# Kernel optimization log

Hardware: AMD Instinct MI355X
Metric: run time of the kernel (lower is better)

## Reference

```python
import jax, jax.numpy as jnp
import numpy as np
import math

B, N, EPG = 64, 1000, 16000          # graphs, nodes/graph, edges/graph
F_IN, H1, H2, C = 128, 128, 64, 10
RATIO = 0.8
K_PROP = 2


def setup_inputs():
    key = jax.random.key(0)
    ks = jax.random.split(key, 24)
    x = jax.random.normal(ks[0], (B * N, F_IN), jnp.float32)
    # edges generated within each graph, then offset to global node ids
    e = jax.random.randint(ks[1], (2, B, EPG), 0, N, dtype=jnp.int32)
    e = e + (jnp.arange(B, dtype=jnp.int32) * N)[None, :, None]
    out = {"x": x, "src": e[0].reshape(-1), "dst": e[1].reshape(-1)}

    def lin(k, fan_in, fan_out):
        s = 1.0 / math.sqrt(fan_in)
        kw, kb = jax.random.split(k)
        return (jax.random.uniform(kw, (fan_in, fan_out), jnp.float32, -s, s),
                jax.random.uniform(kb, (fan_out,), jnp.float32, -s, s))

    dims = [("11", F_IN, H1), ("12", F_IN, H1), ("13", F_IN, H1),
            ("21", H1, H1), ("22", H1, H1), ("23", H1, H1),
            ("31", H1, H1), ("32", H1, H1), ("33", H1, H1),
            ("1", 2 * H1, H1), ("2", H1, H2), ("3", H2, C)]
    for i, (nm, di, do) in enumerate(dims):
        w, b = lin(ks[2 + i], di, do)
        out["w" + nm] = w
        out["b" + nm] = b
    for i in range(3):
        out["p%d" % (i + 1)] = jax.random.normal(ks[20 + i], (H1,), jnp.float32)
    return out


def gcn_prop(h, src, dst, emask, n):
    # GCN symmetric norm with self-loops; emask zeroes filtered edges
    deg = jnp.zeros((n,), h.dtype).at[dst].add(emask) + 1.0
    dinv = jax.lax.rsqrt(deg)
    coef = dinv[src] * dinv[dst] * emask                      # [E]
    out = jnp.zeros_like(h).at[dst].add(h[src] * coef[:, None])
    return out + h * (dinv * dinv)[:, None]                   # self-loop term


def gra_inc(h, src, dst, emask):
    # Gra_inc(K): K incremental propagation steps h <- h + A_hat h
    for _ in range(K_PROP):
        h = h + gcn_prop(h, src, dst, emask, h.shape[0])
    return h


def topk_pool(x, src, dst, emask, p, n_per_graph):
    # PyG TopKPooling: score = x.p/||p||, keep top ceil(ratio*n) per graph,
    # gate kept features by tanh(score), filter & remap edges.
    k = int(math.ceil(RATIO * n_per_graph))
    score = x @ p / jnp.linalg.norm(p)                        # [B*n]
    idx = jax.lax.top_k(score.reshape(B, n_per_graph), k)[1]  # [B,k] local
    perm = (idx + (jnp.arange(B, dtype=idx.dtype) * n_per_graph)[:, None]).reshape(-1)
    new_x = x[perm] * jnp.tanh(score[perm])[:, None]
    remap = jnp.full((B * n_per_graph,), -1, jnp.int32).at[perm].set(
        jnp.arange(B * k, dtype=jnp.int32))
    ns, nd = remap[src], remap[dst]
    valid = emask * ((ns >= 0) & (nd >= 0)).astype(x.dtype)
    return new_x, jnp.maximum(ns, 0), jnp.maximum(nd, 0), valid, k


def readout(x, k):
    xg = x.reshape(B, k, H1)
    return jnp.concatenate([xg.max(axis=1), xg.mean(axis=1)], axis=-1)  # [B,2H]


def reference(x, src, dst, w11, b11, w12, b12, w13, b13, w21, b21, w22, b22,
              w23, b23, w31, b31, w32, b32, w33, b33, w1, b1, w2, b2, w3, b3,
              p1, p2, p3):
    emask = jnp.ones((src.shape[0],), x.dtype)
    n = N
    reads = []
    for (wa, ba), (wb, bb), (wc, bc), p in [
            ((w11, b11), (w12, b12), (w13, b13), p1),
            ((w21, b21), (w22, b22), (w23, b23), p2),
            ((w31, b31), (w32, b32), (w33, b33), p3)]:
        h = (gra_inc(jax.nn.relu(x @ wa + ba), src, dst, emask)
             + gra_inc(jax.nn.relu(x @ wb + bb), src, dst, emask)
             + gra_inc(jax.nn.relu(x @ wc + bc), src, dst, emask))
        x, src, dst, emask, n = topk_pool(h, src, dst, emask, p, n)
        reads.append(readout(x, n))
    z = reads[0] + reads[1] + reads[2]
    z = jax.nn.relu(z @ w1 + b1)
    z = jax.nn.relu(z @ w2 + b2)  # dropout identity in eval mode
    return jax.nn.log_softmax(z @ w3 + b3, axis=-1)
```

## Files before the change

### kernel.cpp

```cpp
#include <hip/hip_runtime.h>
#include <hip/hip_bf16.h>
#include <math.h>

#define BGR 64
#define ECAP 16000
#define EMAX 1024000

typedef _Float16 f16x8 __attribute__((ext_vector_type(8)));
typedef float f32x4 __attribute__((ext_vector_type(4)));

__global__ __launch_bounds__(128) void pnorm3_kernel(const float* __restrict__ p1,
                              const float* __restrict__ p2,
                              const float* __restrict__ p3, float* __restrict__ out) {
    __shared__ float buf[128];
    int t = threadIdx.x, b = blockIdx.x;
    const float* p = (b == 0) ? p1 : (b == 1) ? p2 : p3;
    buf[t] = p[t] * p[t];
    __syncthreads();
    for (int off = 64; off; off >>= 1) {
        if (t < off) buf[t] += buf[t + off];
        __syncthreads();
    }
    if (t == 0) out[b] = sqrtf(buf[0]);
}

struct WP { const float* w[9]; };

__global__ void wsplit_kernel(WP wp, _Float16* __restrict__ out) {
    int mat = blockIdx.x;
    const float* __restrict__ w = wp.w[mat];
    _Float16* __restrict__ dst = out + (size_t)mat * 32768;
    for (int e = threadIdx.x; e < 2048; e += 256) {
        int n = e >> 4;
        int kb = (e & 15) * 8;
        f16x8 hi, lo;
#pragma unroll
        for (int j = 0; j < 8; j++) {
            float v = w[(kb + j) * 128 + n];
            _Float16 h = (_Float16)v;
            hi[j] = h;
            lo[j] = (_Float16)((v - (float)h) * 2048.0f);
        }
        int ks = kb >> 5, kg = (kb >> 3) & 3;
        *(f16x8*)(dst + ((((ks * 2 + 0) * 4 + kg) * 128 + n) * 8)) = hi;
        *(f16x8*)(dst + ((((ks * 2 + 1) * 4 + kg) * 128 + n) * 8)) = lo;
    }
}

__global__ __launch_bounds__(1024) void build_kernel(
    const int* __restrict__ src, const int* __restrict__ dst,
    const int* __restrict__ gcnt, int fixedcnt, int npg,
    int2* __restrict__ rowdeg, float* __restrict__ dinv, int2* __restrict__ edata) {
    __shared__ int cnt[1024];
    __shared__ int scn[1024];
    __shared__ float sdinv[1024];
    int g = blockIdx.x, t = threadIdx.x;
    int E = gcnt ? gcnt[g] : fixedcnt;
    int ebase = g * ECAP;
    int gnb = g * npg;
    cnt[t] = 0;
    __syncthreads();
    for (int i = t; i < E; i += 1024)
        atomicAdd(&cnt[dst[ebase + i] - gnb], 1);
    __syncthreads();
    int myc = (t < npg) ? cnt[t] : 0;
    scn[t] = myc;
    __syncthreads();
    for (int off = 1; off < 1024; off <<= 1) {
        int v = (t >= off) ? scn[t - off] : 0;
        __syncthreads();
        scn[t] += v;
        __syncthreads();
    }
    int excl = scn[t] - myc;
    if (t < npg) {
        float dv = rsqrtf((float)myc + 1.0f);
        rowdeg[gnb + t] = make_int2(ebase + excl, myc);
        dinv[gnb + t] = dv;
        sdinv[t] = dv;
        scn[t] = excl;
    }
    __syncthreads();
    for (int i = t; i < E; i += 1024) {
        int s = src[ebase + i];
        int d = dst[ebase + i];
        int sl = s - gnb, dl = d - gnb;
        int pos = atomicAdd(&scn[dl], 1);
        edata[ebase + pos] = make_int2(s, __float_as_int(sdinv[sl] * sdinv[dl]));
    }
}

__global__ __launch_bounds__(256) void gemm3m_kernel(
    const float* __restrict__ x, const _Float16* __restrict__ wsp,
    const float* __restrict__ b0, const float* __restrict__ b1, const float* __restrict__ b2,
    float* __restrict__ out) {
    __shared__ _Float16 ws[2][16384] __attribute__((aligned(16)));
    const int tid = threadIdx.x;
    const int wave = tid >> 6;
    const int lane = tid & 63;
    const int l15 = lane & 15;
    const int kg = lane >> 4;
    const long base = (long)blockIdx.x * 64;
    const int m = wave * 16 + l15;

    float4 xrow[8];
    const float4* xg = (const float4*)(x + (base + m) * 128);
#pragma unroll
    for (int q = 0; q < 8; q++) xrow[q] = xg[(q >> 1) * 8 + kg * 2 + (q & 1)];

    auto stageH = [&](int s, int buf) {
#pragma unroll
        for (int t = 0; t < 8; t++) {
            int u = tid + t * 256;
            __builtin_amdgcn_global_load_lds(
                (const __attribute__((address_space(1))) unsigned int*)(wsp + (size_t)s * 16384 + u * 8),
                (__attribute__((address_space(3))) unsigned int*)(&ws[buf][u * 8]),
                16, 0, 0);
        }
    };

    float tot[8][4];
#pragma unroll
    for (int nt = 0; nt < 8; nt++)
#pragma unroll
        for (int r = 0; r < 4; r++) tot[nt][r] = 0.f;

    f32x4 acc_h[8], acc_m[8];
    stageH(0, 0);

    for (int s = 0; s < 6; s++) {
        const int j = s >> 1;
        __syncthreads();
        if (s < 5) stageH(s + 1, (s & 1) ^ 1);

        if ((s & 1) == 0) {
#pragma unroll
            for (int nt = 0; nt < 8; nt++) {
                acc_h[nt] = (f32x4){0.f, 0.f, 0.f, 0.f};
                acc_m[nt] = (f32x4){0.f, 0.f, 0.f, 0.f};
            }
        }

        const _Float16* wbase = &ws[s & 1][0];
#pragma unroll
        for (int ksl = 0; ksl < 2; ksl++) {
            const int ks = (s & 1) * 2 + ksl;
            float ev[8] = {xrow[ks * 2].x, xrow[ks * 2].y, xrow[ks * 2].z, xrow[ks * 2].w,
                           xrow[ks * 2 + 1].x, xrow[ks * 2 + 1].y, xrow[ks * 2 + 1].z, xrow[ks * 2 + 1].w};
            f16x8 ah, al;
#pragma unroll
            for (int i = 0; i < 8; i++) {
                _Float16 h = (_Float16)ev[i];
                ah[i] = h;
                al[i] = (_Float16)((ev[i] - (float)h) * 2048.0f);
            }
            const _Float16* wb = wbase + ksl * 8192;
            const int nb = kg * 1024 + l15 * 8;
            f16x8 bh[8], bl[8];
#pragma unroll
            for (int nt = 0; nt < 8; nt++) {
                bh[nt] = *(const f16x8*)(wb + nb + nt * 128);
                bl[nt] = *(const f16x8*)(wb + 4096 + nb + nt * 128);
            }
#pragma unroll
            for (int nt = 0; nt < 8; nt++)
                acc_h[nt] = __builtin_amdgcn_mfma_f32_16x16x32_f16(ah, bh[nt], acc_h[nt], 0, 0, 0);
#pragma unroll
            for (int nt = 0; nt < 8; nt++)
                acc_m[nt] = __builtin_amdgcn_mfma_f32_16x16x32_f16(ah, bl[nt], acc_m[nt], 0, 0, 0);
#pragma unroll
            for (int nt = 0; nt < 8; nt++)
                acc_m[nt] = __builtin_amdgcn_mfma_f32_16x16x32_f16(al, bh[nt], acc_m[nt], 0, 0, 0);
        }

        if (s & 1) {
            const float* bb = (j == 0) ? b0 : (j == 1) ? b1 : b2;
#pragma unroll
            for (int nt = 0; nt < 8; nt++) {
                float bv = bb[nt * 16 + l15];
#pragma unroll
                for (int r = 0; r < 4; r++)
                    tot[nt][r] += fmaxf(acc_h[nt][r] + acc_m[nt][r] * (1.0f / 2048.0f) + bv, 0.f);
            }
        }
    }

    float* op = out + (base + wave * 16 + kg * 4) * 128 + l15;
#pragma unroll
    for (int nt = 0; nt < 8; nt++)
#pragma unroll
        for (int r = 0; r < 4; r++) op[r * 128 + nt * 16] = tot[nt][r];
}

template <int SC>
__global__ __launch_bounds__(256, 4) void prop_t(
    const float* __restrict__ hin, float* __restrict__ hout,
    const int2* __restrict__ rowdeg, const int2* __restrict__ edata,
    const float* __restrict__ dinv,
    const float* __restrict__ p, const float* __restrict__ pn, float* __restrict__ score) {
    int per = gridDim.x >> 3;
    int b = blockIdx.x;
    int sb = (b & 7) * per + (b >> 3);
    int wave = threadIdx.x >> 6;
    int lane = threadIdx.x & 63;
    int half = lane >> 5;
    int l31 = lane & 31;
    int node = sb * 8 + wave * 2 + half;

    const char* hb = (const char*)hin;
    const unsigned loff = (unsigned)l31 * 16u;

    float4 hv = *(const float4*)(hb + (size_t)node * 512 + loff);
    float di = dinv[node];
    float selfc = 1.0f + di * di;
    float ax = hv.x * selfc, ay = hv.y * selfc, az = hv.z * selfc, aw = hv.w * selfc;

    int2 rd = rowdeg[node];
    int e0 = rd.x;
    int dg = rd.y;
    int e1 = e0 + dg;
    int degA = __builtin_amdgcn_readlane(dg, 0);
    int degB = __builtin_amdgcn_readlane(dg, 32);
    int dmax = degA > degB ? degA : degB;
    int T = (dmax + 15) >> 4;

    for (int t = 0; t < T; ++t) {
        int ee = e0 + t * 16 + (lane & 15);
        int ec = ee < e1 - 1 ? ee : e1 - 1;
        ec = ec < e0 ? e0 : ec;
        int2 md = edata[ec];
        bool val = ee < e1;
        int ci = val ? md.x : 0;
        int wi = val ? md.y : 0;
        float4 g[16];
        float w[16];
#pragma unroll
        for (int j = 0; j < 16; ++j) {
            int iA = __builtin_amdgcn_readlane(ci, j);
            int iB = __builtin_amdgcn_readlane(ci, j + 32);
            float wA = __int_as_float(__builtin_amdgcn_readlane(wi, j));
            float wB = __int_as_float(__builtin_amdgcn_readlane(wi, j + 32));
            int idx = half ? iB : iA;
            w[j] = half ? wB : wA;
            g[j] = *(const float4*)(hb + (unsigned)idx * 512u + loff);
        }
        __builtin_amdgcn_sched_barrier(0);
#pragma unroll
        for (int j = 0; j < 16; ++j) {
            ax += w[j] * g[j].x;
            ay += w[j] * g[j].y;
            az += w[j] * g[j].z;
            aw += w[j] * g[j].w;
        }
    }

    *(float4*)((char*)hout + (size_t)node * 512 + loff) = make_float4(ax, ay, az, aw);

    if (SC) {
        float4 pv = ((const float4*)p)[l31];
        float v = ax * pv.x + ay * pv.y + az * pv.z + aw * pv.w;
        v += __shfl_xor(v, 16);
        v += __shfl_xor(v, 8);
        v += __shfl_xor(v, 4);
        v += __shfl_xor(v, 2);
        v += __shfl_xor(v, 1);
        if (l31 == 0) score[node] = v / pn[0];
    }
}

__global__ __launch_bounds__(1024) void pool_kernel(const float* __restrict__ score, int npg, int k,
                            int* __restrict__ perm, float* __restrict__ gate,
                            int* __restrict__ remap) {
    __shared__ unsigned long long skey[1024];
    int b = blockIdx.x, t = threadIdx.x;
    float v = (t < npg) ? score[b * npg + t] : -INFINITY;
    unsigned ub = __float_as_uint(v);
    unsigned asc = ub ^ ((ub >> 31) ? 0xFFFFFFFFu : 0x80000000u);
    unsigned desc = ~asc;
    skey[t] = ((unsigned long long)desc << 32) | (unsigned)t;
    __syncthreads();
    for (int ksz = 2; ksz <= 1024; ksz <<= 1) {
        for (int j = ksz >> 1; j > 0; j >>= 1) {
            int l = t ^ j;
            if (l > t) {
                unsigned long long a = skey[t], c = skey[l];
                bool up = ((t & ksz) == 0);
                if (up ? (a > c) : (a < c)) { skey[t] = c; skey[l] = a; }
            }
            __syncthreads();
        }
    }
    if (t < k) {
        int idx = (int)(skey[t] & 0xFFFFFFFFu);
        int oldg = b * npg + idx;
        int newg = b * k + t;
        perm[newg] = oldg;
        gate[newg] = tanhf(score[oldg]);
        remap[oldg] = newg;
    } else if (t < npg) {
        int idx = (int)(skey[t] & 0xFFFFFFFFu);
        remap[b * npg + idx] = -1;
    }
}

__global__ void newx_kernel(const float* __restrict__ h, const int* __restrict__ perm,
                            const float* __restrict__ gate, float* __restrict__ xo) {
    int m = blockIdx.x * 4 + (threadIdx.x >> 6);
    int lane = threadIdx.x & 63;
    int old = perm[m];
    float g = gate[m];
    float2 v = ((const float2*)h)[old * 64 + lane];
    ((float2*)xo)[m * 64 + lane] = make_float2(v.x * g, v.y * g);
}

__global__ __launch_bounds__(512) void readout_kernel(const float* __restrict__ x,
                                                      float* __restrict__ rsum, int k,
                                                      int first) {
    __shared__ float smx[4][128], ssm[4][128];
    int b = blockIdx.x, t = threadIdx.x;
    int f = t & 127, c = t >> 7;
    int rows = k >> 2;
    const float* base = x + (size_t)b * k * 128 + (size_t)c * rows * 128 + f;
    float mx = -INFINITY, sm = 0.f;
#pragma unroll 8
    for (int j = 0; j < rows; j++) {
        float v = base[(size_t)j * 128];
        mx = fmaxf(mx, v);
        sm += v;
    }
    smx[c][f] = mx;
    ssm[c][f] = sm;
    __syncthreads();
    if (c == 0) {
        float m2 = fmaxf(fmaxf(smx[0][f], smx[1][f]), fmaxf(smx[2][f], smx[3][f]));
        float s2 = (ssm[0][f] + ssm[1][f] + ssm[2][f] + ssm[3][f]) / (float)k;
        if (first) {
            rsum[b * 256 + f] = m2;
            rsum[b * 256 + 128 + f] = s2;
        } else {
            rsum[b * 256 + f] += m2;
            rsum[b * 256 + 128 + f] += s2;
        }
    }
}

__global__ __launch_bounds__(1024) void compact_kernel(
    const int* __restrict__ src, const int* __restrict__ dst,
    const int* __restrict__ gcntIn, int fixedIn, const int* __restrict__ remap,
    int* __restrict__ so, int* __restrict__ dd, int* __restrict__ gcntOut) {
    __shared__ int wsum[16];
    __shared__ int runbase;
    int g = blockIdx.x, t = threadIdx.x;
    int wave = t >> 6, lane = t & 63;
    int E = gcntIn ? gcntIn[g] : fixedIn;
    int ebase = g * ECAP;
    if (t == 0) runbase = 0;
    __syncthreads();
    for (int i0 = 0; i0 < E; i0 += 1024) {
        int i = i0 + t;
        bool v = false;
        int s = 0, d = 0;
        if (i < E) {
            s = remap[src[ebase + i]];
            d = remap[dst[ebase + i]];
            v = ((s | d) >= 0);
        }
        unsigned long long m = __ballot(v);
        int before = __popcll(m & ((1ULL << lane) - 1ULL));
        if (lane == 0) wsum[wave] = __popcll(m);
        __syncthreads();
        if (t == 0) {
            int tot = 0;
#pragma unroll
            for (int w2 = 0; w2 < 16; w2++) { int c = wsum[w2]; wsum[w2] = runbase + tot; tot += c; }
            runbase += tot;
        }
        __syncthreads();
        if (v) {
            int pos = ebase + wsum[wave] + before;
            so[pos] = s;
            dd[pos] = d;
        }
        __syncthreads();
    }
    if (t == 0) gcntOut[g] = runbase;
}

__global__ void mlp_kernel(const float* __restrict__ rsum,
                           const float* __restrict__ w1, const float* __restrict__ b1,
                           const float* __restrict__ w2, const float* __restrict__ b2,
                           const float* __restrict__ w3, const float* __restrict__ b3,
                           float* __restrict__ out) {
    __shared__ float z0[256], z1l[128], z2l[64], lg[10], ls;
    int b = blockIdx.x, t = threadIdx.x;
    z0[t] = rsum[b * 256 + t];
    z0[t + 128] = rsum[b * 256 + 128 + t];
    __syncthreads();
    float acc = b1[t];
    for (int k = 0; k < 256; k++) acc += z0[k] * w1[k * 128 + t];
    z1l[t] = fmaxf(acc, 0.f);
    __syncthreads();
    if (t < 64) {
        acc = b2[t];
        for (int k = 0; k < 128; k++) acc += z1l[k] * w2[k * 64 + t];
        z2l[t] = fmaxf(acc, 0.f);
    }
    __syncthreads();
    if (t < 10) {
        acc = b3[t];
        for (int k = 0; k < 64; k++) acc += z2l[k] * w3[k * 10 + t];
        lg[t] = acc;
    }
    __syncthreads();
    if (t == 0) {
        float mx = lg[0];
        for (int c = 1; c < 10; c++) mx = fmaxf(mx, lg[c]);
        float s = 0.f;
        for (int c = 0; c < 10; c++) s += expf(lg[c] - mx);
        ls = mx + logf(s);
    }
    __syncthreads();
    if (t < 10) out[b * 10 + t] = lg[t] - ls;
}

extern "C" void kernel_launch(void* const* d_in, const int* in_sizes, int n_in,
                              void* d_out, int out_size, void* d_ws, size_t ws_size,
                              hipStream_t stream) {
    char* ws = (char*)d_ws;
    size_t off = 0;
    auto alloc = [&](size_t bytes) -> void* {
        void* p = ws + off;
        off += (bytes + 255) & ~(size_t)255;
        return p;
    };
    float* hA = (float*)alloc(64000UL * 128 * 4);
    float* hB = (float*)alloc(64000UL * 128 * 4);
    float* score = (float*)alloc(64000UL * 4);
    float* dinvb = (float*)alloc(64000UL * 4);
    int2* rowdeg = (int2*)alloc(64000UL * 8);
    int2* edata = (int2*)alloc((size_t)EMAX * 8);
    int* srcA = (int*)alloc((size_t)EMAX * 4);
    int* dstA = (int*)alloc((size_t)EMAX * 4);
    int* srcB = (int*)alloc((size_t)EMAX * 4);
    int* dstB = (int*)alloc((size_t)EMAX * 4);
    int* perm = (int*)alloc(51200UL * 4);
    float* gate = (float*)alloc(51200UL * 4);
    int* remap = (int*)alloc(64000UL * 4);
    float* rsum = (float*)alloc(64UL * 256 * 4);
    _Float16* wsall = (_Float16*)alloc(9UL * 32768 * 2);
    float* pnorm = (float*)alloc(256);
    int* gA = (int*)alloc(256);
    int* gB = (int*)alloc(256);
    (void)ws_size;

    const float* x0 = (const float*)d_in[0];
    const int* src0 = (const int*)d_in[1];
    const int* dst0 = (const int*)d_in[2];

    pnorm3_kernel<<<3, 128, 0, stream>>>((const float*)d_in[27], (const float*)d_in[28],
                                         (const float*)d_in[29], pnorm);

    WP wp;
    wp.w[0] = (const float*)d_in[3];  wp.w[1] = (const float*)d_in[5];  wp.w[2] = (const float*)d_in[7];
    wp.w[3] = (const float*)d_in[9];  wp.w[4] = (const float*)d_in[11]; wp.w[5] = (const float*)d_in[13];
    wp.w[6] = (const float*)d_in[15]; wp.w[7] = (const float*)d_in[17]; wp.w[8] = (const float*)d_in[19];
    wsplit_kernel<<<9, 256, 0, stream>>>(wp, wsall);

    auto run_layer = [&](int n, int npg, int k, const float* x, int layer,
                         const int* esrc, const int* edst, const int* gcnt,
                         const float* ba, const float* bb, const float* bc,
                         const float* p, const float* pn,
                         int* so, int* ddst, int* gout) {
        build_kernel<<<BGR, 1024, 0, stream>>>(esrc, edst, gcnt, ECAP, npg,
                                               rowdeg, dinvb, edata);
        gemm3m_kernel<<<n / 64, 256, 0, stream>>>(x, wsall + (size_t)layer * 3 * 32768,
                                                  ba, bb, bc, hA);
        prop_t<0><<<n / 8, 256, 0, stream>>>(hA, hB, rowdeg, edata, dinvb,
                                             nullptr, nullptr, nullptr);
        prop_t<1><<<n / 8, 256, 0, stream>>>(hB, hA, rowdeg, edata, dinvb,
                                             p, pn, score);
        pool_kernel<<<BGR, 1024, 0, stream>>>(score, npg, k, perm, gate, remap);
        newx_kernel<<<(BGR * k) / 4, 256, 0, stream>>>(hA, perm, gate, hB);
        readout_kernel<<<BGR, 512, 0, stream>>>(hB, rsum, k, layer == 0 ? 1 : 0);
        if (gout)
            compact_kernel<<<BGR, 1024, 0, stream>>>(esrc, edst, gcnt, ECAP, remap,
                                                     so, ddst, gout);
    };

    run_layer(64000, 1000, 800, x0, 0, src0, dst0, nullptr,
              (const float*)d_in[4], (const float*)d_in[6], (const float*)d_in[8],
              (const float*)d_in[27], pnorm + 0, srcA, dstA, gA);

    run_layer(51200, 800, 640, hB, 1, srcA, dstA, gA,
              (const float*)d_in[10], (const float*)d_in[12], (const float*)d_in[14],
              (const float*)d_in[28], pnorm + 1, srcB, dstB, gB);

    run_layer(40960, 640, 512, hB, 2, srcB, dstB, gB,
              (const float*)d_in[16], (const float*)d_in[18], (const float*)d_in[20],
              (const float*)d_in[29], pnorm + 2, nullptr, nullptr, nullptr);

    mlp_kernel<<<64, 128, 0, stream>>>(rsum, (const float*)d_in[21], (const float*)d_in[22],
                                       (const float*)d_in[23], (const float*)d_in[24],
                                       (const float*)d_in[25], (const float*)d_in[26],
                                       (float*)d_out);
}
```

Before: 448.4 us.

## Fuse pooled gather with readout and use bpermute for edge index broadcast

Merges the gather-and-gate kernel into the readout kernel, so each pooled row is gathered, scaled by tanh(score), stored and reduced in one pass. This saves a kernel launch and a re-read of the pooled features. In the propagation loop, four readlanes plus selects per edge are replaced by two ds_bpermute ops that broadcast each half-wave's edge index and weight. The fused kernel runs only 64 blocks with a non-unrolled dependent gather loop, which may lower parallelism and latency hiding. bpermute goes through the LDS crossbar rather than scalar registers.

```diff
diff --git a/kernel.cpp b/kernel.cpp
--- a/kernel.cpp
+++ b/kernel.cpp
@@ -206,6 +206,7 @@
     int half = lane >> 5;
     int l31 = lane & 31;
     int node = sb * 8 + wave * 2 + half;
+    int pbase = (lane & 32) << 2;
 
     const char* hb = (const char*)hin;
     const unsigned loff = (unsigned)l31 * 16u;
@@ -236,12 +237,9 @@
         float w[16];
 #pragma unroll
         for (int j = 0; j < 16; ++j) {
-            int iA = __builtin_amdgcn_readlane(ci, j);
-            int iB = __builtin_amdgcn_readlane(ci, j + 32);
-            float wA = __int_as_float(__builtin_amdgcn_readlane(wi, j));
-            float wB = __int_as_float(__builtin_amdgcn_readlane(wi, j + 32));
-            int idx = half ? iB : iA;
-            w[j] = half ? wB : wA;
+            int idx = __builtin_amdgcn_ds_bpermute(pbase + j * 4, ci);
+            int wj = __builtin_amdgcn_ds_bpermute(pbase + j * 4, wi);
+            w[j] = __int_as_float(wj);
             g[j] = *(const float4*)(hb + (unsigned)idx * 512u + loff);
         }
         __builtin_amdgcn_sched_barrier(0);
@@ -303,28 +301,22 @@
     }
 }
 
-__global__ void newx_kernel(const float* __restrict__ h, const int* __restrict__ perm,
-                            const float* __restrict__ gate, float* __restrict__ xo) {
-    int m = blockIdx.x * 4 + (threadIdx.x >> 6);
-    int lane = threadIdx.x & 63;
-    int old = perm[m];
-    float g = gate[m];
-    float2 v = ((const float2*)h)[old * 64 + lane];
-    ((float2*)xo)[m * 64 + lane] = make_float2(v.x * g, v.y * g);
-}
-
-__global__ __launch_bounds__(512) void readout_kernel(const float* __restrict__ x,
-                                                      float* __restrict__ rsum, int k,
-                                                      int first) {
+__global__ __launch_bounds__(512) void newxread_kernel(
+    const float* __restrict__ h, const int* __restrict__ perm,
+    const float* __restrict__ gate, float* __restrict__ xo,
+    float* __restrict__ rsum, int k, int first) {
     __shared__ float smx[4][128], ssm[4][128];
     int b = blockIdx.x, t = threadIdx.x;
     int f = t & 127, c = t >> 7;
     int rows = k >> 2;
-    const float* base = x + (size_t)b * k * 128 + (size_t)c * rows * 128 + f;
+    int r0 = c * rows;
     float mx = -INFINITY, sm = 0.f;
-#pragma unroll 8
     for (int j = 0; j < rows; j++) {
-        float v = base[(size_t)j * 128];
+        int m = b * k + r0 + j;
+        int old = perm[m];
+        float g = gate[m];
+        float v = h[(size_t)old * 128 + f] * g;
+        xo[(size_t)m * 128 + f] = v;
         mx = fmaxf(mx, v);
         sm += v;
     }
@@ -480,8 +472,8 @@
         prop_t<1><<<n / 8, 256, 0, stream>>>(hB, hA, rowdeg, edata, dinvb,
                                              p, pn, score);
         pool_kernel<<<BGR, 1024, 0, stream>>>(score, npg, k, perm, gate, remap);
-        newx_kernel<<<(BGR * k) / 4, 256, 0, stream>>>(hA, perm, gate, hB);
-        readout_kernel<<<BGR, 512, 0, stream>>>(hB, rsum, k, layer == 0 ? 1 : 0);
+        newxread_kernel<<<BGR, 512, 0, stream>>>(hA, perm, gate, hB, rsum, k,
+                                                 layer == 0 ? 1 : 0);
         if (gout)
             compact_kernel<<<BGR, 1024, 0, stream>>>(esrc, edst, gcnt, ECAP, remap,
                                                      so, ddst, gout);
```

New measurement: 659.8 us. +47.2%, slower.
